# Kernel optimization log

Hardware: AMD Instinct MI355X
Metric: run time of the kernel (lower is better)

## Reference

```python
import jax, jax.numpy as jnp
import numpy as np

D_MODEL, N_LEVELS, N_HEADS, N_POINTS = 256, 4, 8, 4
HEAD_DIM = D_MODEL // N_HEADS
SPATIAL = [(100, 100), (50, 50), (25, 25), (13, 13)]  # (H, W) per level
BATCH = 2


def setup_inputs() -> dict:
    key = jax.random.key(0)
    ks = jax.random.split(key, 10)
    len_in = sum(h * w for h, w in SPATIAL)
    n, lq = BATCH, len_in
    s = 0.02
    mlp = N_HEADS * N_LEVELS * N_POINTS
    starts = np.cumsum([0] + [h * w for h, w in SPATIAL])[:-1]
    return {
        "query": jax.random.normal(ks[0], (n, lq, D_MODEL), jnp.float32),
        "reference_points": jax.random.uniform(ks[1], (n, lq, N_LEVELS, 2), jnp.float32),
        "input_flatten": jax.random.normal(ks[2], (n, len_in, D_MODEL), jnp.float32),
        "input_spatial_shapes": jnp.array(SPATIAL, dtype=jnp.int32),
        "input_level_start_index": jnp.array(starts, dtype=jnp.int32),
        "Wv": jax.random.normal(ks[3], (D_MODEL, D_MODEL), jnp.float32) * s,
        "bv": jnp.zeros((D_MODEL,), jnp.float32),
        "Woff": jax.random.normal(ks[4], (D_MODEL, mlp * 2), jnp.float32) * s,
        "boff": jax.random.normal(ks[5], (mlp * 2,), jnp.float32) * s,
        "Wattn": jax.random.normal(ks[6], (D_MODEL, mlp), jnp.float32) * s,
        "battn": jnp.zeros((mlp,), jnp.float32),
        "Wout": jax.random.normal(ks[7], (D_MODEL, D_MODEL), jnp.float32) * s,
        "bout": jnp.zeros((D_MODEL,), jnp.float32),
    }


def _ms_deform_attn_core(value, spatial_shapes, loc, aw):
    """value [N,S,M,D]; loc [N,Lq,M,L,P,2] in [0,1]; aw [N,Lq,M,L,P] -> [N,Lq,M*D].
    Faithful to F.grid_sample(mode='bilinear', padding_mode='zeros', align_corners=False)."""
    n, lq, m, L, p, _ = loc.shape
    d = value.shape[-1]
    out = jnp.zeros((n, m, lq, d), value.dtype)
    gather = jax.vmap(jax.vmap(lambda v, i: v[i]))  # vmap over N and M
    start = 0
    for lvl, (H, W) in enumerate(spatial_shapes):
        v = value[:, start:start + H * W].transpose(0, 2, 1, 3)  # [N,M,HW,D]
        start += H * W
        # align_corners=False: grid g=2*loc-1 -> pixel = ((g+1)*size-1)/2 = loc*size-0.5
        x = loc[:, :, :, lvl, :, 0] * W - 0.5  # [N,Lq,M,P]
        y = loc[:, :, :, lvl, :, 1] * H - 0.5
        x0 = jnp.floor(x)
        y0 = jnp.floor(y)
        wx = x - x0
        wy = y - y0
        x0i = x0.astype(jnp.int32)
        y0i = y0.astype(jnp.int32)
        samp = jnp.zeros((n, m, lq * p, d), value.dtype)
        for dy, wyc in ((0, 1.0 - wy), (1, wy)):
            for dx, wxc in ((0, 1.0 - wx), (1, wx)):
                xi = x0i + dx
                yi = y0i + dy
                valid = (xi >= 0) & (xi < W) & (yi >= 0) & (yi < H)  # zeros padding
                idx = jnp.clip(yi, 0, H - 1) * W + jnp.clip(xi, 0, W - 1)
                idx = idx.transpose(0, 2, 1, 3).reshape(n, m, lq * p)
                w = (wxc * wyc * valid).transpose(0, 2, 1, 3).reshape(n, m, lq * p)
                samp = samp + gather(v, idx) * w[..., None]
        samp = samp.reshape(n, m, lq, p, d)
        aw_l = aw[:, :, :, lvl, :].transpose(0, 2, 1, 3)  # [N,M,Lq,P]
        out = out + (samp * aw_l[..., None]).sum(3)
    return out.transpose(0, 2, 1, 3).reshape(n, lq, m * d)


def reference(query, reference_points, input_flatten, input_spatial_shapes,
              input_level_start_index, Wv, bv, Woff, boff, Wattn, battn, Wout, bout):
    n, lq, _ = query.shape
    m, L, p = N_HEADS, N_LEVELS, N_POINTS
    shapes = np.asarray(input_spatial_shapes)  # concrete/static [L,2] = (H,W)
    value = (input_flatten @ Wv + bv).reshape(n, -1, m, HEAD_DIM)
    off = (query @ Woff + boff).reshape(n, lq, m, L, p, 2)
    aw = jax.nn.softmax((query @ Wattn + battn).reshape(n, lq, m, L * p), axis=-1)
    aw = aw.reshape(n, lq, m, L, p)
    norm = jnp.asarray(shapes[:, ::-1].astype(np.float32))  # [L,2] = (W,H)
    loc = reference_points[:, :, None, :, None, :] + off / norm[None, None, None, :, None, :]
    out = _ms_deform_attn_core(value, [tuple(s) for s in shapes.tolist()], loc, aw)
    return out @ Wout + bout
```

## Files before the change

### kernel.cpp

```cpp
#include <hip/hip_runtime.h>
#include <hip/hip_bf16.h>

#define NB    2
#define LQ    13294
#define DM    256
#define NH    8
#define HD    32
#define NL    4
#define NP    4
#define ROWS  (NB*LQ)

#define OFF_VALUE 0u
#define OFF_TMP   13613056u
#define OFF_OFFS  27226112u
#define OFF_AWL   54452224u
#define OFF_WT    61258752u
#define OFF_FLAG  61717504u

#define WT_WV    0
#define WT_WOFF  65536
#define WT_WATTN 131072
#define WT_WOUT  163840

typedef __attribute__((ext_vector_type(8))) short short8;
typedef __attribute__((ext_vector_type(4))) float floatx4;

static __device__ __forceinline__ float blo(int u)  { return __uint_as_float(((unsigned)u) << 16); }
static __device__ __forceinline__ float bhif(int u) { return __uint_as_float(((unsigned)u) & 0xffff0000u); }

static __device__ __forceinline__ int pack_bf2(float a, float b) {
    __hip_bfloat162 h(__float2bfloat16(a), __float2bfloat16(b));
    int u; __builtin_memcpy(&u, &h, 4); return u;
}

static __device__ __forceinline__ void gload_lds16(const void* g, void* l) {
    __builtin_amdgcn_global_load_lds(
        (const __attribute__((address_space(1))) unsigned*)g,
        (__attribute__((address_space(3))) unsigned*)l, 16, 0, 0);
}

__global__ void sniff_k(const unsigned int* __restrict__ q, int* __restrict__ flag) {
    const int t = threadIdx.x;
    int hits = 0;
#pragma unroll
    for (int i = 0; i < 4; ++i) {
        unsigned lo = q[t * 4 + i] & 0xffffu;
        unsigned e  = (lo >> 7) & 0xffu;
        if ((e >= 110u && e <= 132u) || lo == 0u) ++hits;
    }
#pragma unroll
    for (int s = 1; s < 64; s <<= 1) hits += __shfl_xor(hits, s);
    if (t == 0) *flag = (hits > 160) ? 1 : 0;
}

__global__ __launch_bounds__(256) void trans_k(
    const void* __restrict__ s0, const void* __restrict__ s1,
    const void* __restrict__ s2, const void* __restrict__ s3,
    short* __restrict__ wt, const int* __restrict__ flagp)
{
    const int flag = *flagp;
    const int z = blockIdx.z;
    const void* src = (z == 0) ? s0 : (z == 1) ? s1 : (z == 2) ? s2 : s3;
    short* dst = wt + ((z == 0) ? WT_WV : (z == 1) ? WT_WOFF : (z == 2) ? WT_WATTN : WT_WOUT);
    const int N = (z == 2) ? 128 : 256;
    const int n0 = blockIdx.x * 32, k0 = blockIdx.y * 32;
    if (n0 >= N) return;

    __shared__ short tile[32 * 36];
    const int t = threadIdx.x;
    const int r = t >> 3, c4 = (t & 7) * 4;
    if (flag) {
        const short* sp = (const short*)src + (k0 + r) * N + n0 + c4;
        *(short4*)&tile[r * 36 + c4] = *(const short4*)sp;
    } else {
        const float* sp = (const float*)src + (k0 + r) * N + n0 + c4;
        float4 v = *(const float4*)sp;
        short4 o;
        o.x = (short)(pack_bf2(v.x, v.x) & 0xffff);
        o.y = (short)(pack_bf2(v.y, v.y) & 0xffff);
        o.z = (short)(pack_bf2(v.z, v.z) & 0xffff);
        o.w = (short)(pack_bf2(v.w, v.w) & 0xffff);
        *(short4*)&tile[r * 36 + c4] = o;
    }
    __syncthreads();
    const int nn = t >> 3, r4 = (t & 7) * 4;
    short4 o;
    o.x = tile[(r4 + 0) * 36 + nn];
    o.y = tile[(r4 + 1) * 36 + nn];
    o.z = tile[(r4 + 2) * 36 + nn];
    o.w = tile[(r4 + 3) * 36 + nn];
    *(short4*)&dst[(n0 + nn) * 256 + k0 + r4] = o;
}

__global__ __launch_bounds__(256) void gemm_lds_k(
    const void* __restrict__ A, const short* __restrict__ Wt,
    const void* __restrict__ bias, const void* __restrict__ bias2,
    void* __restrict__ C, void* __restrict__ C2,
    int M, int Nn, int a_mode, int c_mode, const int* __restrict__ flagp)
{
    const int  flag = *flagp;
    const bool a_bf = (a_mode == 2) ? (flag != 0) : true;

    __shared__ __align__(16) short As[128 * 32];
    __shared__ __align__(16) short Bs[128 * 32];

    const int tid = threadIdx.x;
    const int w = tid >> 6, lane = tid & 63;
    const int qd = lane >> 4, ln = lane & 15;
    const int bm = blockIdx.y * 128, bn = blockIdx.x * 128;
    const int wm = (w & 1) * 64, wn = (w >> 1) * 64;

    const int ar0 = tid >> 2,        ak0 = (tid & 3) * 8;
    const int ar1 = (tid + 256) >> 2, ak1 = (tid & 3) * 8;
    const int ga0 = min(bm + ar0, M - 1), ga1 = min(bm + ar1, M - 1);
    short* lA0 = As + w * 512;
    short* lA1 = As + 2048 + w * 512;
    short* lB0 = Bs + w * 512;
    short* lB1 = Bs + 2048 + w * 512;

    floatx4 acc[4][4];
#pragma unroll
    for (int i = 0; i < 4; ++i)
#pragma unroll
        for (int j = 0; j < 4; ++j) acc[i][j] = floatx4{0.f, 0.f, 0.f, 0.f};

    const short* Ab = (const short*)A;
    const float* Af = (const float*)A;

    for (int k0 = 0; k0 < 256; k0 += 32) {
        __syncthreads();
        gload_lds16(Wt + (bn + ar0) * 256 + k0 + ak0, lB0);
        gload_lds16(Wt + (bn + ar1) * 256 + k0 + ak1, lB1);
        if (a_bf) {
            gload_lds16(Ab + ga0 * 256 + k0 + ak0, lA0);
            gload_lds16(Ab + ga1 * 256 + k0 + ak1, lA1);
        } else {
            float4 f0 = *(const float4*)(Af + ga0 * 256 + k0 + ak0);
            float4 f1 = *(const float4*)(Af + ga0 * 256 + k0 + ak0 + 4);
            int4 p0; p0.x = pack_bf2(f0.x, f0.y); p0.y = pack_bf2(f0.z, f0.w);
                     p0.z = pack_bf2(f1.x, f1.y); p0.w = pack_bf2(f1.z, f1.w);
            *(int4*)&As[ar0 * 32 + ak0] = p0;
            float4 g0 = *(const float4*)(Af + ga1 * 256 + k0 + ak1);
            float4 g1 = *(const float4*)(Af + ga1 * 256 + k0 + ak1 + 4);
            int4 p1; p1.x = pack_bf2(g0.x, g0.y); p1.y = pack_bf2(g0.z, g0.w);
                     p1.z = pack_bf2(g1.x, g1.y); p1.w = pack_bf2(g1.z, g1.w);
            *(int4*)&As[ar1 * 32 + ak1] = p1;
        }
        __syncthreads();

        short8 af[4], bf[4];
#pragma unroll
        for (int i = 0; i < 4; ++i)
            af[i] = *(const short8*)&As[(wm + i * 16 + ln) * 32 + qd * 8];
#pragma unroll
        for (int j = 0; j < 4; ++j)
            bf[j] = *(const short8*)&Bs[(wn + j * 16 + ln) * 32 + qd * 8];
#pragma unroll
        for (int i = 0; i < 4; ++i)
#pragma unroll
            for (int j = 0; j < 4; ++j)
                acc[i][j] = __builtin_amdgcn_mfma_f32_16x16x32_bf16(af[i], bf[j], acc[i][j], 0, 0, 0);
    }

#pragma unroll
    for (int j = 0; j < 4; ++j) {
        const int col = bn + wn + j * 16 + ln;
        float bj;
        if (c_mode == 3 && col >= 256) {
            if (flag) bj = __bfloat162float(((const __hip_bfloat16*)bias2)[col - 256]);
            else      bj = ((const float*)bias2)[col - 256];
        } else {
            if (flag) bj = __bfloat162float(((const __hip_bfloat16*)bias)[col]);
            else      bj = ((const float*)bias)[col];
        }
#pragma unroll
        for (int i = 0; i < 4; ++i) {
#pragma unroll
            for (int r = 0; r < 4; ++r) {
                const int row = bm + wm + i * 16 + qd * 4 + r;
                if (row >= M) continue;
                const float v = acc[i][j][r] + bj;
                if (c_mode == 0)      ((__hip_bfloat16*)C)[row * Nn + col] = __float2bfloat16(v);
                else if (c_mode == 1) ((float*)C)[row * Nn + col] = v;
                else if (c_mode == 2) {
                    if (flag) ((__hip_bfloat16*)C)[row * Nn + col] = __float2bfloat16(v);
                    else      ((float*)C)[row * Nn + col] = v;
                } else {
                    if (col < 256) ((float*)C)[row * 256 + col] = v;
                    else           ((__hip_bfloat16*)C2)[row * 128 + col - 256] = __float2bfloat16(v);
                }
            }
        }
    }
}

__global__ __launch_bounds__(256) void sampler_k(
    const void* __restrict__ refp, const short* __restrict__ value,
    const float* __restrict__ offs, const short* __restrict__ awl,
    short* __restrict__ tmp, const int* __restrict__ flagp)
{
    const int flag = *flagp;
    const int wq = threadIdx.x >> 6;
    const int nq = blockIdx.x * 4 + wq;
    const int lane = threadIdx.x & 63;
    const int h = lane >> 3, u = lane & 7;
    const int n = (nq >= LQ) ? 1 : 0;

    __shared__ int2 recs[4][16][9][4];

    const int lg = *(const int*)(awl + nq * 128 + h * 16 + u * 2);
    float l0 = blo(lg), l1 = bhif(lg);
    float m = fmaxf(l0, l1);
    m = fmaxf(m, __shfl_xor(m, 1));
    m = fmaxf(m, __shfl_xor(m, 2));
    m = fmaxf(m, __shfl_xor(m, 4));
    float e0 = __expf(l0 - m), e1 = __expf(l1 - m);
    float s = e0 + e1;
    s += __shfl_xor(s, 1);
    s += __shfl_xor(s, 2);
    s += __shfl_xor(s, 4);
    const float inv = 1.f / s;
    const float w0 = e0 * inv, w1 = e1 * inv;

    const float4 of = *(const float4*)(offs + nq * 256 + h * 32 + u * 4);

    float rxl, ryl;
    if (flag) {
        const int rr = *(const int*)((const short*)refp + nq * 8 + (u & 3) * 2);
        rxl = blo(rr); ryl = bhif(rr);
    } else {
        const float* rp = (const float*)refp + nq * 8 + (u & 3) * 2;
        rxl = rp[0]; ryl = rp[1];
    }

    const int l = u >> 1;
    const int Wl = (0x0D193264 >> (l * 8)) & 0xff;
    const int St = (l == 0) ? 0 : (l == 1) ? 10000 : (l == 2) ? 12500 : 13125;
    const int rowbase = n * LQ + St;
    const float Wf = (float)Wl;
    const float rx = __shfl(rxl, h * 8 + l);
    const float ry = __shfl(ryl, h * 8 + l);

#pragma unroll
    for (int j = 0; j < 2; ++j) {
        const float ox = j ? of.z : of.x;
        const float oy = j ? of.w : of.y;
        const float wa = j ? w1 : w0;
        const float px = fmaf(rx, Wf, ox) - 0.5f;
        const float py = fmaf(ry, Wf, oy) - 0.5f;
        const float x0f = floorf(px), y0f = floorf(py);
        const float wx = px - x0f, wy = py - y0f;
        const int x0 = (int)x0f, y0 = (int)y0f;
        const float wxc[2] = {1.f - wx, wx};
        const float wyc[2] = {1.f - wy, wy};
#pragma unroll
        for (int dy = 0; dy < 2; ++dy) {
#pragma unroll
            for (int dx = 0; dx < 2; ++dx) {
                const int xi = x0 + dx, yi = y0 + dy;
                const bool vld = ((unsigned)xi < (unsigned)Wl) & ((unsigned)yi < (unsigned)Wl);
                int row = rowbase + yi * Wl + xi;
                row = vld ? row : rowbase;
                const float ww = vld ? wa * wxc[dx] * wyc[dy] : 0.f;
                recs[wq][u * 2 + j][h][dy * 2 + dx] =
                    make_int2(row << 9, __float_as_int(ww));
            }
        }
    }

    __syncthreads();

    const int laneoff = h * 64 + u * 8;
    const char* vb = (const char*)value;
    float a0 = 0.f, a1 = 0.f, a2 = 0.f, a3 = 0.f;

#pragma unroll
    for (int idx = 0; idx < 16; ++idx) {
#pragma unroll
        for (int c = 0; c < 4; ++c) {
            const int2 r = recs[wq][idx][h][c];
            const float w = __int_as_float(r.y);
            const int2 raw = *(const int2*)(vb + (unsigned)(r.x + laneoff));
            a0 = fmaf(w, blo(raw.x),  a0);
            a1 = fmaf(w, bhif(raw.x), a1);
            a2 = fmaf(w, blo(raw.y),  a2);
            a3 = fmaf(w, bhif(raw.y), a3);
        }
    }

    int2 o;
    o.x = pack_bf2(a0, a1);
    o.y = pack_bf2(a2, a3);
    *(int2*)(tmp + nq * 256 + h * 32 + u * 4) = o;
}

extern "C" void kernel_launch(void* const* d_in, const int* in_sizes, int n_in,
                              void* d_out, int out_size, void* d_ws, size_t ws_size,
                              hipStream_t stream)
{
    const void* query  = d_in[0];
    const void* refpts = d_in[1];
    const void* flat   = d_in[2];
    const void* Wv     = d_in[5];
    const void* bv     = d_in[6];
    const void* Woff   = d_in[7];
    const void* boff   = d_in[8];
    const void* Wattn  = d_in[9];
    const void* battn  = d_in[10];
    const void* Wout   = d_in[11];
    const void* bout   = d_in[12];

    char* ws = (char*)d_ws;
    short* value = (short*)(ws + OFF_VALUE);
    short* tmp   = (short*)(ws + OFF_TMP);
    float* offsb = (float*)(ws + OFF_OFFS);
    short* awl   = (short*)(ws + OFF_AWL);
    short* wt    = (short*)(ws + OFF_WT);
    int*   flagp = (int*)(ws + OFF_FLAG);

    const int gmy = (ROWS + 127) / 128;

    sniff_k<<<1, 64, 0, stream>>>((const unsigned int*)query, flagp);
    trans_k<<<dim3(8, 8, 4), 256, 0, stream>>>(Wv, Woff, Wattn, Wout, wt, flagp);
    gemm_lds_k<<<dim3(2, gmy), 256, 0, stream>>>(flat, wt + WT_WV, bv, nullptr,
                                                 value, nullptr, ROWS, 256, 2, 0, flagp);
    gemm_lds_k<<<dim3(3, gmy), 256, 0, stream>>>(query, wt + WT_WOFF, boff, battn,
                                                 offsb, awl, ROWS, 384, 2, 3, flagp);
    sampler_k<<<ROWS / 4, 256, 0, stream>>>(refpts, value, offsb, awl, tmp, flagp);
    gemm_lds_k<<<dim3(2, gmy), 256, 0, stream>>>(tmp, wt + WT_WOUT, bout, nullptr,
                                                 d_out, nullptr, ROWS, 256, 1, 2, flagp);
}
```

Baseline: 238.0 us.

## Merge value and offset GEMMs into one launch; software-pipeline sampler gathers

The value projection and the offset/attention projection GEMMs now run as one launch, using blockIdx.z to choose the problem. This removes a launch and lets both GEMMs share the GPU, with wasted early-exit blocks on the smaller half. The sampler's gather loop becomes a two-buffer scheme that issues eight loads ahead of consumption, to hide global memory latency at the cost of more registers. Its LDS record array is also padded in the last dimension to reduce bank conflicts.

```diff
diff --git a/kernel.cpp b/kernel.cpp
--- a/kernel.cpp
+++ b/kernel.cpp
@@ -92,25 +92,21 @@
     *(short4*)&dst[(n0 + nn) * 256 + k0 + r4] = o;
 }
 
-__global__ __launch_bounds__(256) void gemm_lds_k(
+static __device__ __forceinline__ void gemm_body(
     const void* __restrict__ A, const short* __restrict__ Wt,
     const void* __restrict__ bias, const void* __restrict__ bias2,
     void* __restrict__ C, void* __restrict__ C2,
-    int M, int Nn, int a_mode, int c_mode, const int* __restrict__ flagp)
-{
-    const int  flag = *flagp;
-    const bool a_bf = (a_mode == 2) ? (flag != 0) : true;
-
-    __shared__ __align__(16) short As[128 * 32];
-    __shared__ __align__(16) short Bs[128 * 32];
-
+    const int M, const int Nn, const bool a_bf, const int c_mode,
+    const int flag, const int bx, const int by,
+    short* __restrict__ As, short* __restrict__ Bs)
+{
     const int tid = threadIdx.x;
     const int w = tid >> 6, lane = tid & 63;
     const int qd = lane >> 4, ln = lane & 15;
-    const int bm = blockIdx.y * 128, bn = blockIdx.x * 128;
+    const int bm = by * 128, bn = bx * 128;
     const int wm = (w & 1) * 64, wn = (w >> 1) * 64;
 
-    const int ar0 = tid >> 2,        ak0 = (tid & 3) * 8;
+    const int ar0 = tid >> 2,         ak0 = (tid & 3) * 8;
     const int ar1 = (tid + 256) >> 2, ak1 = (tid & 3) * 8;
     const int ga0 = min(bm + ar0, M - 1), ga1 = min(bm + ar1, M - 1);
     short* lA0 = As + w * 512;
@@ -194,6 +190,42 @@
     }
 }
 
+__global__ __launch_bounds__(256) void gemm_lds_k(
+    const void* __restrict__ A, const short* __restrict__ Wt,
+    const void* __restrict__ bias, const void* __restrict__ bias2,
+    void* __restrict__ C, void* __restrict__ C2,
+    int M, int Nn, int a_mode, int c_mode, const int* __restrict__ flagp)
+{
+    __shared__ __align__(16) short As[128 * 32];
+    __shared__ __align__(16) short Bs[128 * 32];
+    const int flag = *flagp;
+    const bool a_bf = (a_mode == 2) ? (flag != 0) : true;
+    gemm_body(A, Wt, bias, bias2, C, C2, M, Nn, a_bf, c_mode, flag,
+              blockIdx.x, blockIdx.y, As, Bs);
+}
+
+__global__ __launch_bounds__(256) void gemm_fused_k(
+    const void* __restrict__ flat, const void* __restrict__ query,
+    const short* __restrict__ wt,
+    const void* __restrict__ bv, const void* __restrict__ boff,
+    const void* __restrict__ battn,
+    void* __restrict__ value, void* __restrict__ offsb, void* __restrict__ awl,
+    const int* __restrict__ flagp)
+{
+    __shared__ __align__(16) short As[128 * 32];
+    __shared__ __align__(16) short Bs[128 * 32];
+    const int flag = *flagp;
+    const bool a_bf = (flag != 0);
+    if (blockIdx.z == 0) {
+        if (blockIdx.x >= 2) return;
+        gemm_body(flat, wt + WT_WV, bv, nullptr, value, nullptr,
+                  ROWS, 256, a_bf, 0, flag, blockIdx.x, blockIdx.y, As, Bs);
+    } else {
+        gemm_body(query, wt + WT_WOFF, boff, battn, offsb, awl,
+                  ROWS, 384, a_bf, 3, flag, blockIdx.x, blockIdx.y, As, Bs);
+    }
+}
+
 __global__ __launch_bounds__(256) void sampler_k(
     const void* __restrict__ refp, const short* __restrict__ value,
     const float* __restrict__ offs, const short* __restrict__ awl,
@@ -206,7 +238,7 @@
     const int h = lane >> 3, u = lane & 7;
     const int n = (nq >= LQ) ? 1 : 0;
 
-    __shared__ int2 recs[4][16][9][4];
+    __shared__ int2 recs[4][16][9][5];
 
     const int lg = *(const int*)(awl + nq * 128 + h * 16 + u * 2);
     float l0 = blo(lg), l1 = bhif(lg);
@@ -274,19 +306,37 @@
     const char* vb = (const char*)value;
     float a0 = 0.f, a1 = 0.f, a2 = 0.f, a3 = 0.f;
 
-#pragma unroll
-    for (int idx = 0; idx < 16; ++idx) {
-#pragma unroll
-        for (int c = 0; c < 4; ++c) {
-            const int2 r = recs[wq][idx][h][c];
-            const float w = __int_as_float(r.y);
-            const int2 raw = *(const int2*)(vb + (unsigned)(r.x + laneoff));
-            a0 = fmaf(w, blo(raw.x),  a0);
-            a1 = fmaf(w, bhif(raw.x), a1);
-            a2 = fmaf(w, blo(raw.y),  a2);
-            a3 = fmaf(w, bhif(raw.y), a3);
-        }
-    }
+    int2  rA[8], rB[8];
+    float wA[8], wB[8];
+
+#define CHUNK(RW, WW, kk)                                                 \
+    _Pragma("unroll")                                                     \
+    for (int j = 0; j < 8; ++j) {                                         \
+        const int2 rr = recs[wq][(kk) * 2 + (j >> 2)][h][j & 3];          \
+        WW[j] = __int_as_float(rr.y);                                     \
+        RW[j] = *(const int2*)(vb + (unsigned)(rr.x + laneoff));          \
+    }
+#define EAT(RW, WW)                                                       \
+    _Pragma("unroll")                                                     \
+    for (int j = 0; j < 8; ++j) {                                         \
+        a0 = fmaf(WW[j], blo(RW[j].x),  a0);                              \
+        a1 = fmaf(WW[j], bhif(RW[j].x), a1);                              \
+        a2 = fmaf(WW[j], blo(RW[j].y),  a2);                              \
+        a3 = fmaf(WW[j], bhif(RW[j].y), a3);                              \
+    }
+
+    CHUNK(rA, wA, 0)
+    CHUNK(rB, wB, 1)
+    EAT(rA, wA)  CHUNK(rA, wA, 2)
+    EAT(rB, wB)  CHUNK(rB, wB, 3)
+    EAT(rA, wA)  CHUNK(rA, wA, 4)
+    EAT(rB, wB)  CHUNK(rB, wB, 5)
+    EAT(rA, wA)  CHUNK(rA, wA, 6)
+    EAT(rB, wB)  CHUNK(rB, wB, 7)
+    EAT(rA, wA)
+    EAT(rB, wB)
+#undef CHUNK
+#undef EAT
 
     int2 o;
     o.x = pack_bf2(a0, a1);
@@ -322,10 +372,8 @@
 
     sniff_k<<<1, 64, 0, stream>>>((const unsigned int*)query, flagp);
     trans_k<<<dim3(8, 8, 4), 256, 0, stream>>>(Wv, Woff, Wattn, Wout, wt, flagp);
-    gemm_lds_k<<<dim3(2, gmy), 256, 0, stream>>>(flat, wt + WT_WV, bv, nullptr,
-                                                 value, nullptr, ROWS, 256, 2, 0, flagp);
-    gemm_lds_k<<<dim3(3, gmy), 256, 0, stream>>>(query, wt + WT_WOFF, boff, battn,
-                                                 offsb, awl, ROWS, 384, 2, 3, flagp);
+    gemm_fused_k<<<dim3(3, gmy, 2), 256, 0, stream>>>(flat, query, wt, bv, boff, battn,
+                                                      value, offsb, awl, flagp);
     sampler_k<<<ROWS / 4, 256, 0, stream>>>(refpts, value, offsb, awl, tmp, flagp);
     gemm_lds_k<<<dim3(2, gmy), 256, 0, stream>>>(tmp, wt + WT_WOUT, bout, nullptr,
                                                  d_out, nullptr, ROWS, 256, 1, 2, flagp);
```

Result: faster. 229.3 us (-3.7%).
